# Kernel optimization log

Hardware: AMD Instinct MI355X
Metric: run time of the kernel (lower is better)

Reference implementation:

```python
import jax, jax.numpy as jnp
import numpy as np

N_NODES = 50000


def _gcn_norm(edge_index, num_nodes):
    # PyG gcn_norm with add_self_loops=True, edge_weight=1
    src = jnp.concatenate([edge_index[0], jnp.arange(num_nodes, dtype=edge_index.dtype)])
    dst = jnp.concatenate([edge_index[1], jnp.arange(num_nodes, dtype=edge_index.dtype)])
    deg = jax.ops.segment_sum(jnp.ones_like(dst, dtype=jnp.float32), dst,
                              num_segments=num_nodes)
    deg_inv_sqrt = jnp.where(deg > 0, jax.lax.rsqrt(deg), 0.0)
    norm = deg_inv_sqrt[src] * deg_inv_sqrt[dst]  # [E + N]
    return src, dst, norm


def _gcn_conv(x, src, dst, norm, W, b, num_nodes):
    h = x @ W                                   # [N, F_out] linear first
    msg = h[src] * norm[:, None]                # gather + scale  [E+N, F_out]
    out = jax.ops.segment_sum(msg, dst, num_segments=num_nodes)  # scatter-add
    return out + b


def setup_inputs() -> dict:
    key = jax.random.key(0)
    k1, k2, k3, k4 = jax.random.split(key, 4)
    IN_C, HID, OUT_C, E = 128, 96, 48, 800000
    x = jax.random.normal(k1, (N_NODES, IN_C), dtype=jnp.float32)
    edge_index = jax.random.randint(k2, (2, E), 0, N_NODES, dtype=jnp.int64)
    # Glorot-style scaled weights
    W1 = jax.random.normal(k3, (IN_C, HID), dtype=jnp.float32) * (1.0 / np.sqrt(IN_C))
    b1 = jnp.zeros((HID,), dtype=jnp.float32)
    W2 = jax.random.normal(k4, (HID, OUT_C), dtype=jnp.float32) * (1.0 / np.sqrt(HID))
    b2 = jnp.zeros((OUT_C,), dtype=jnp.float32)
    return {"x": x, "edge_index": edge_index, "W1": W1, "b1": b1, "W2": W2, "b2": b2}


def reference(x, edge_index, W1, b1, W2, b2):
    # cached=True: normalization computed once and reused by both layers
    src, dst, norm = _gcn_norm(edge_index, N_NODES)
    h = jax.nn.relu(_gcn_conv(x, src, dst, norm, W1, b1, N_NODES))
    return _gcn_conv(h, src, dst, norm, W2, b2, N_NODES)
```

## Files before the change

### kernel.cpp

```cpp
#include <hip/hip_runtime.h>

static constexpr int IN_C  = 128;
static constexpr int HID   = 96;
static constexpr int OUT_C = 48;

static constexpr int NPART     = 8;
static constexpr int FILL_ITER = 16;
static constexpr int CHUNK     = 256 * FILL_ITER;

typedef short bf16x8 __attribute__((ext_vector_type(8)));
typedef float f32x4  __attribute__((ext_vector_type(4)));


__device__ __forceinline__ unsigned short f2bf(float f) {
  union { float f; unsigned u; } c; c.f = f;
  unsigned r = c.u + 0x7fffu + ((c.u >> 16) & 1u);
  return (unsigned short)(r >> 16);
}
__device__ __forceinline__ float bflo(unsigned u) {
  union { unsigned u; float f; } c; c.u = u << 16; return c.f;
}
__device__ __forceinline__ float bfhi(unsigned u) {
  union { unsigned u; float f; } c; c.u = u & 0xffff0000u; return c.f;
}


__global__ void k_zero(int* __restrict__ p, int n) {
  int i = blockIdx.x * blockDim.x + threadIdx.x;
  if (i < n) p[i] = 0;
}

__device__ __forceinline__ void wprep_one(const float* W, uint4* Wt,
                                          int K, int M, int idx) {
  int lane = idx & 63;
  int t = idx >> 6;
  int KB = K / 32;
  int c  = t / KB;
  int kb = t - c * KB;
  int col = c * 16 + (lane & 15);
  int k0  = kb * 32 + (lane >> 4) * 8;
  unsigned pk[4];
#pragma unroll
  for (int q = 0; q < 4; ++q) {
    unsigned lo = f2bf(W[(size_t)(k0 + 2 * q) * M + col]);
    unsigned hi = f2bf(W[(size_t)(k0 + 2 * q + 1) * M + col]);
    pk[q] = lo | (hi << 16);
  }
  Wt[idx] = make_uint4(pk[0], pk[1], pk[2], pk[3]);
}

__global__ void k_wprep(const float* __restrict__ W1, uint4* __restrict__ Wt1, int T1,
                        const float* __restrict__ W2, uint4* __restrict__ Wt2, int T2) {
  int idx = blockIdx.x * blockDim.x + threadIdx.x;
  if (idx < T1) wprep_one(W1, Wt1, IN_C, HID, idx);
  else if (idx < T1 + T2) wprep_one(W2, Wt2, HID, OUT_C, idx - T1);
}


__global__ void k_count(const int* __restrict__ dst, int* __restrict__ cnt,
                        int* __restrict__ perm, int E) {
  int e = blockIdx.x * blockDim.x + threadIdx.x;
  if (e < E) perm[e] = atomicAdd(&cnt[dst[e]], 1);
}

__global__ void k_scan_block(const int* __restrict__ in, int* __restrict__ out_excl,
                             int* __restrict__ bsum, int n) {
  __shared__ int sm[256];
  int i = blockIdx.x * 256 + threadIdx.x;
  int v = (i < n) ? in[i] : 0;
  int val = v;
  sm[threadIdx.x] = val;
  __syncthreads();
  for (int off = 1; off < 256; off <<= 1) {
    int t = (threadIdx.x >= (unsigned)off) ? sm[threadIdx.x - off] : 0;
    __syncthreads();
    val += t;
    sm[threadIdx.x] = val;
    __syncthreads();
  }
  if (i < n) out_excl[i] = val - v;
  if (threadIdx.x == 255) bsum[blockIdx.x] = val;
}

__global__ void k_finish(int* __restrict__ rs, const int* __restrict__ boff,
                         const int* __restrict__ cnt,
                         float* __restrict__ dinv, int n) {
  int i = blockIdx.x * 256 + threadIdx.x;
  if (i >= n) return;
  rs[i] = rs[i] + boff[blockIdx.x];
  dinv[i] = rsqrtf((float)cnt[i] + 1.0f);
}

__global__ __launch_bounds__(256) void k_fill_part(
    const int* __restrict__ src, const int* __restrict__ dst,
    const int* __restrict__ perm, const int* __restrict__ rs,
    int* __restrict__ csr, int E, int P) {
  int lo = blockIdx.x * P;
  int hi = lo + P;
  int base = blockIdx.y * CHUNK + threadIdx.x;
#pragma unroll
  for (int i = 0; i < FILL_ITER; ++i) {
    int e = base + i * 256;
    if (e < E) {
      int d = dst[e];
      if (d >= lo && d < hi) {
        csr[rs[d] + perm[e]] = src[e];
      }
    }
  }
}


template <int K, int M, bool ABF16>
__global__ __launch_bounds__(256) void k_gemm(const void* __restrict__ Xv,
                                              const uint4* __restrict__ Wt,
                                              const float* __restrict__ dinv,
                                              unsigned short* __restrict__ Y,
                                              int N) {
  constexpr int KB = K / 32;
  constexpr int CT = M / 16;
  constexpr int GR = K / 8;
  __shared__ unsigned short lds[64 * 128];
  const int tid  = threadIdx.x;
  const int base = blockIdx.x * 64;

  for (int idx = tid; idx < 64 * GR; idx += 256) {
    int row = idx / GR;
    int g   = idx - row * GR;
    int srow = min(base + row, N - 1);
    uint4 pk;
    if (ABF16) {
      pk = *(const uint4*)((const unsigned short*)Xv + (size_t)srow * K + g * 8);
    } else {
      const float* xp = (const float*)Xv + (size_t)srow * K + g * 8;
      float4 v0 = *(const float4*)xp;
      float4 v1 = *(const float4*)(xp + 4);
      pk.x = (unsigned)f2bf(v0.x) | ((unsigned)f2bf(v0.y) << 16);
      pk.y = (unsigned)f2bf(v0.z) | ((unsigned)f2bf(v0.w) << 16);
      pk.z = (unsigned)f2bf(v1.x) | ((unsigned)f2bf(v1.y) << 16);
      pk.w = (unsigned)f2bf(v1.z) | ((unsigned)f2bf(v1.w) << 16);
    }
    int gs = g ^ (row & 7);
    *(uint4*)(&lds[row * 128 + gs * 8]) = pk;
  }
  __syncthreads();

  const int lane = tid & 63;
  const int wv   = tid >> 6;
  const int lrow = wv * 16 + (lane & 15);
  const int khi  = lane >> 4;

  f32x4 acc[CT];
#pragma unroll
  for (int c = 0; c < CT; ++c) acc[c] = (f32x4){0.f, 0.f, 0.f, 0.f};

  const bf16x8* Wb = (const bf16x8*)Wt;
#pragma unroll
  for (int kb = 0; kb < KB; ++kb) {
    int j  = khi + kb * 4;
    int js = j ^ (lrow & 7);
    bf16x8 a = *(const bf16x8*)(&lds[lrow * 128 + js * 8]);
#pragma unroll
    for (int c = 0; c < CT; ++c) {
      bf16x8 b = Wb[(c * KB + kb) * 64 + lane];
      acc[c] = __builtin_amdgcn_mfma_f32_16x16x32_bf16(a, b, acc[c], 0, 0, 0);
    }
  }

  const int r0 = base + wv * 16 + khi * 4;
#pragma unroll
  for (int i = 0; i < 4; ++i) {
    int row = r0 + i;
    if (row < N) {
      float d = dinv[row];
      unsigned short* yp = Y + (size_t)row * M + (lane & 15);
#pragma unroll
      for (int c = 0; c < CT; ++c) {
        yp[c * 16] = f2bf(acc[c][i] * d);
      }
    }
  }
}


__device__ __forceinline__ void bfacc(float* a, const uint4& v) {
  a[0] += bflo(v.x); a[1] += bfhi(v.x);
  a[2] += bflo(v.y); a[3] += bfhi(v.y);
  a[4] += bflo(v.z); a[5] += bfhi(v.z);
  a[6] += bflo(v.w); a[7] += bfhi(v.w);
}

template <int M, bool RELU, bool OBF16>
__global__ __launch_bounds__(256) void k_agg(const unsigned short* __restrict__ Hs,
                                             const int* __restrict__ csr,
                                             const int* __restrict__ rs,
                                             const int* __restrict__ cnt,
                                             const float* __restrict__ dinv,
                                             const float* __restrict__ bias,
                                             void* __restrict__ outv, int N) {
  constexpr int JC = M / 8;
  int gid = blockIdx.x * blockDim.x + threadIdx.x;
  int n = gid / JC;
  if (n >= N) return;
  int f8 = (gid - n * JC) * 8;
  float dn = dinv[n];
  float a[8] = {};
  {
    uint4 sv = *(const uint4*)(Hs + (size_t)n * M + f8);
    bfacc(a, sv);
  }
  int p = rs[n];
  int e = cnt[n];
  int i = 0;
  for (; i + 4 <= e; i += 4) {
    int s0 = csr[p + i];
    int s1 = csr[p + i + 1];
    int s2 = csr[p + i + 2];
    int s3 = csr[p + i + 3];
    uint4 g0 = *(const uint4*)(Hs + (size_t)s0 * M + f8);
    uint4 g1 = *(const uint4*)(Hs + (size_t)s1 * M + f8);
    uint4 g2 = *(const uint4*)(Hs + (size_t)s2 * M + f8);
    uint4 g3 = *(const uint4*)(Hs + (size_t)s3 * M + f8);
    bfacc(a, g0); bfacc(a, g1); bfacc(a, g2); bfacc(a, g3);
  }
  for (; i < e; ++i) {
    int s = csr[p + i];
    uint4 g = *(const uint4*)(Hs + (size_t)s * M + f8);
    bfacc(a, g);
  }
  float r[8];
#pragma unroll
  for (int q = 0; q < 8; ++q) {
    r[q] = fmaf(dn, a[q], bias[f8 + q]);
    if (RELU) r[q] = fmaxf(r[q], 0.0f);
  }
  if (OBF16) {
    uint4 pk;
    pk.x = (unsigned)f2bf(r[0]) | ((unsigned)f2bf(r[1]) << 16);
    pk.y = (unsigned)f2bf(r[2]) | ((unsigned)f2bf(r[3]) << 16);
    pk.z = (unsigned)f2bf(r[4]) | ((unsigned)f2bf(r[5]) << 16);
    pk.w = (unsigned)f2bf(r[6]) | ((unsigned)f2bf(r[7]) << 16);
    *(uint4*)((unsigned short*)outv + (size_t)n * M + f8) = pk;
  } else {
    float* op = (float*)outv + (size_t)n * M + f8;
    *(float4*)(op)     = make_float4(r[0], r[1], r[2], r[3]);
    *(float4*)(op + 4) = make_float4(r[4], r[5], r[6], r[7]);
  }
}


extern "C" void kernel_launch(void* const* d_in, const int* in_sizes, int n_in,
                              void* d_out, int out_size, void* d_ws, size_t ws_size,
                              hipStream_t stream) {
  const float* x  = (const float*)d_in[0];
  const int*   ei = (const int*)d_in[1];
  const float* W1 = (const float*)d_in[2];
  const float* b1 = (const float*)d_in[3];
  const float* W2 = (const float*)d_in[4];
  const float* b2 = (const float*)d_in[5];
  float* out = (float*)d_out;

  const int N = in_sizes[0] / IN_C;
  const int E = in_sizes[1] / 2;
  const int* src = ei;
  const int* dst = ei + E;

  char* ws = (char*)d_ws;
  size_t off = 0;
  auto alloc = [&](size_t bytes) -> void* {
    void* p = ws + off;
    off = (off + bytes + 255) & ~(size_t)255;
    return p;
  };
  int*   cnt    = (int*)alloc((size_t)N * 4);
  int*   rs     = (int*)alloc((size_t)N * 4);
  float* dinv   = (float*)alloc((size_t)N * 4);
  int*   bsum   = (int*)alloc(256 * 4);
  int*   boff   = (int*)alloc(256 * 4);
  int*   junk   = (int*)alloc(256 * 4);
  int*   perm   = (int*)alloc((size_t)E * 4);
  int*   csr    = (int*)alloc((size_t)E * 4);
  unsigned short* hbf = (unsigned short*)alloc((size_t)N * HID * 2);
  unsigned short* hb2 = (unsigned short*)alloc((size_t)N * HID * 2);
  constexpr int T1 = (HID / 16) * (IN_C / 32) * 64;
  constexpr int T2 = (OUT_C / 16) * (HID / 32) * 64;
  uint4* Wt1 = (uint4*)alloc((size_t)T1 * 16);
  uint4* Wt2 = (uint4*)alloc((size_t)T2 * 16);

  const int nbN = (N + 255) / 256;
  const int nbE = (E + 255) / 256;
  const int P   = (N + NPART - 1) / NPART;

  k_zero<<<nbN, 256, 0, stream>>>(cnt, N);
  k_wprep<<<(T1 + T2 + 255) / 256, 256, 0, stream>>>(W1, Wt1, T1, W2, Wt2, T2);
  k_count<<<nbE, 256, 0, stream>>>(dst, cnt, perm, E);
  k_scan_block<<<nbN, 256, 0, stream>>>(cnt, rs, bsum, N);
  k_scan_block<<<1, 256, 0, stream>>>(bsum, boff, junk, nbN);
  k_finish<<<nbN, 256, 0, stream>>>(rs, boff, cnt, dinv, N);
  dim3 fg(NPART, (E + CHUNK - 1) / CHUNK);
  k_fill_part<<<fg, 256, 0, stream>>>(src, dst, perm, rs, csr, E, P);

  const int rowBlocks = (N + 63) / 64;

  {
    k_gemm<IN_C, HID, false><<<rowBlocks, 256, 0, stream>>>(x, Wt1, dinv, hbf, N);
    int t = N * (HID / 8);
    k_agg<HID, true, true><<<(t + 255) / 256, 256, 0, stream>>>(hbf, csr, rs, cnt, dinv, b1, hb2, N);
  }
  {
    k_gemm<HID, OUT_C, true><<<rowBlocks, 256, 0, stream>>>(hb2, Wt2, dinv, hbf, N);
    int t = N * (OUT_C / 8);
    k_agg<OUT_C, false, false><<<(t + 255) / 256, 256, 0, stream>>>(hbf, csr, rs, cnt, dinv, b2, out, N);
  }
}
```

Baseline: 131.7 us.

## Build CSR with partitioned atomic cursors instead of per-edge perm array

Merges the zeroing and weight-prep kernels into one launch. Replaces the global per-edge atomic count that also recorded a slot index with a destination-partitioned count kernel, and has the fill pass claim CSR slots with atomics on a cursor array. This removes the perm array's write and read traffic and makes atomics partition-local for cache locality. The aggregation gather loop is also unrolled to 8 neighbours for more memory-level parallelism. Neighbour order within a row becomes nondeterministic, which can slightly change floating-point summation order.

```diff
diff --git a/kernel.cpp b/kernel.cpp
--- a/kernel.cpp
+++ b/kernel.cpp
@@ -22,12 +22,6 @@
 }
 __device__ __forceinline__ float bfhi(unsigned u) {
   union { unsigned u; float f; } c; c.u = u & 0xffff0000u; return c.f;
-}
-
-
-__global__ void k_zero(int* __restrict__ p, int n) {
-  int i = blockIdx.x * blockDim.x + threadIdx.x;
-  if (i < n) p[i] = 0;
 }
 
 __device__ __forceinline__ void wprep_one(const float* W, uint4* Wt,
@@ -49,18 +43,34 @@
   Wt[idx] = make_uint4(pk[0], pk[1], pk[2], pk[3]);
 }
 
-__global__ void k_wprep(const float* __restrict__ W1, uint4* __restrict__ Wt1, int T1,
-                        const float* __restrict__ W2, uint4* __restrict__ Wt2, int T2) {
-  int idx = blockIdx.x * blockDim.x + threadIdx.x;
-  if (idx < T1) wprep_one(W1, Wt1, IN_C, HID, idx);
-  else if (idx < T1 + T2) wprep_one(W2, Wt2, HID, OUT_C, idx - T1);
-}
-
-
-__global__ void k_count(const int* __restrict__ dst, int* __restrict__ cnt,
-                        int* __restrict__ perm, int E) {
-  int e = blockIdx.x * blockDim.x + threadIdx.x;
-  if (e < E) perm[e] = atomicAdd(&cnt[dst[e]], 1);
+__global__ void k_init(int* __restrict__ cnt, int n, int nbN,
+                       const float* __restrict__ W1, uint4* __restrict__ Wt1, int T1,
+                       const float* __restrict__ W2, uint4* __restrict__ Wt2, int T2) {
+  int b = blockIdx.x;
+  if (b < nbN) {
+    int i = b * 256 + threadIdx.x;
+    if (i < n) cnt[i] = 0;
+  } else {
+    int idx = (b - nbN) * 256 + threadIdx.x;
+    if (idx < T1) wprep_one(W1, Wt1, IN_C, HID, idx);
+    else if (idx < T1 + T2) wprep_one(W2, Wt2, HID, OUT_C, idx - T1);
+  }
+}
+
+
+__global__ __launch_bounds__(256) void k_count_part(
+    const int* __restrict__ dst, int* __restrict__ cnt, int E, int P) {
+  int lo = blockIdx.x * P;
+  int hi = lo + P;
+  int base = blockIdx.y * CHUNK + threadIdx.x;
+#pragma unroll
+  for (int i = 0; i < FILL_ITER; ++i) {
+    int e = base + i * 256;
+    if (e < E) {
+      int d = dst[e];
+      if (d >= lo && d < hi) atomicAdd(&cnt[d], 1);
+    }
+  }
 }
 
 __global__ void k_scan_block(const int* __restrict__ in, int* __restrict__ out_excl,
@@ -83,18 +93,19 @@
 }
 
 __global__ void k_finish(int* __restrict__ rs, const int* __restrict__ boff,
-                         const int* __restrict__ cnt,
+                         int* __restrict__ cursor, const int* __restrict__ cnt,
                          float* __restrict__ dinv, int n) {
   int i = blockIdx.x * 256 + threadIdx.x;
   if (i >= n) return;
-  rs[i] = rs[i] + boff[blockIdx.x];
+  int r = rs[i] + boff[blockIdx.x];
+  rs[i] = r;
+  cursor[i] = r;
   dinv[i] = rsqrtf((float)cnt[i] + 1.0f);
 }
 
 __global__ __launch_bounds__(256) void k_fill_part(
     const int* __restrict__ src, const int* __restrict__ dst,
-    const int* __restrict__ perm, const int* __restrict__ rs,
-    int* __restrict__ csr, int E, int P) {
+    int* __restrict__ cursor, int* __restrict__ csr, int E, int P) {
   int lo = blockIdx.x * P;
   int hi = lo + P;
   int base = blockIdx.y * CHUNK + threadIdx.x;
@@ -104,7 +115,8 @@
     if (e < E) {
       int d = dst[e];
       if (d >= lo && d < hi) {
-        csr[rs[d] + perm[e]] = src[e];
+        int p = atomicAdd(&cursor[d], 1);
+        csr[p] = src[e];
       }
     }
   }
@@ -212,6 +224,26 @@
   int p = rs[n];
   int e = cnt[n];
   int i = 0;
+  for (; i + 8 <= e; i += 8) {
+    int s0 = csr[p + i];
+    int s1 = csr[p + i + 1];
+    int s2 = csr[p + i + 2];
+    int s3 = csr[p + i + 3];
+    int s4 = csr[p + i + 4];
+    int s5 = csr[p + i + 5];
+    int s6 = csr[p + i + 6];
+    int s7 = csr[p + i + 7];
+    uint4 g0 = *(const uint4*)(Hs + (size_t)s0 * M + f8);
+    uint4 g1 = *(const uint4*)(Hs + (size_t)s1 * M + f8);
+    uint4 g2 = *(const uint4*)(Hs + (size_t)s2 * M + f8);
+    uint4 g3 = *(const uint4*)(Hs + (size_t)s3 * M + f8);
+    uint4 g4 = *(const uint4*)(Hs + (size_t)s4 * M + f8);
+    uint4 g5 = *(const uint4*)(Hs + (size_t)s5 * M + f8);
+    uint4 g6 = *(const uint4*)(Hs + (size_t)s6 * M + f8);
+    uint4 g7 = *(const uint4*)(Hs + (size_t)s7 * M + f8);
+    bfacc(a, g0); bfacc(a, g1); bfacc(a, g2); bfacc(a, g3);
+    bfacc(a, g4); bfacc(a, g5); bfacc(a, g6); bfacc(a, g7);
+  }
   for (; i + 4 <= e; i += 4) {
     int s0 = csr[p + i];
     int s1 = csr[p + i + 1];
@@ -274,11 +306,11 @@
   };
   int*   cnt    = (int*)alloc((size_t)N * 4);
   int*   rs     = (int*)alloc((size_t)N * 4);
+  int*   cursor = (int*)alloc((size_t)N * 4);
   float* dinv   = (float*)alloc((size_t)N * 4);
   int*   bsum   = (int*)alloc(256 * 4);
   int*   boff   = (int*)alloc(256 * 4);
   int*   junk   = (int*)alloc(256 * 4);
-  int*   perm   = (int*)alloc((size_t)E * 4);
   int*   csr    = (int*)alloc((size_t)E * 4);
   unsigned short* hbf = (unsigned short*)alloc((size_t)N * HID * 2);
   unsigned short* hb2 = (unsigned short*)alloc((size_t)N * HID * 2);
@@ -288,17 +320,16 @@
   uint4* Wt2 = (uint4*)alloc((size_t)T2 * 16);
 
   const int nbN = (N + 255) / 256;
-  const int nbE = (E + 255) / 256;
   const int P   = (N + NPART - 1) / NPART;
-
-  k_zero<<<nbN, 256, 0, stream>>>(cnt, N);
-  k_wprep<<<(T1 + T2 + 255) / 256, 256, 0, stream>>>(W1, Wt1, T1, W2, Wt2, T2);
-  k_count<<<nbE, 256, 0, stream>>>(dst, cnt, perm, E);
+  const int wprepBlocks = (T1 + T2 + 255) / 256;
+
+  k_init<<<nbN + wprepBlocks, 256, 0, stream>>>(cnt, N, nbN, W1, Wt1, T1, W2, Wt2, T2);
+  dim3 fg(NPART, (E + CHUNK - 1) / CHUNK);
+  k_count_part<<<fg, 256, 0, stream>>>(dst, cnt, E, P);
   k_scan_block<<<nbN, 256, 0, stream>>>(cnt, rs, bsum, N);
   k_scan_block<<<1, 256, 0, stream>>>(bsum, boff, junk, nbN);
-  k_finish<<<nbN, 256, 0, stream>>>(rs, boff, cnt, dinv, N);
-  dim3 fg(NPART, (E + CHUNK - 1) / CHUNK);
-  k_fill_part<<<fg, 256, 0, stream>>>(src, dst, perm, rs, csr, E, P);
+  k_finish<<<nbN, 256, 0, stream>>>(rs, boff, cursor, cnt, dinv, N);
+  k_fill_part<<<fg, 256, 0, stream>>>(src, dst, cursor, csr, E, P);
 
   const int rowBlocks = (N + 63) / 64;
 
```

Measured after the change: 153.9 us. 16.8% more time.
